# Performance work log

Hardware: AMD Instinct MI355X
Metric: run time of the kernel (lower is better)

Reference implementation:

```python
import jax, jax.numpy as jnp
import numpy as np

N, E, IN_DIM, HID, HEADS = 50000, 800000, 160, 64, 4
NEG_SLOPE = 0.2
BN_EPS = 1e-5


def setup_inputs() -> dict:
    key = jax.random.key(0)
    ks = jax.random.split(key, 32)
    s = lambda i, shape, sc=0.05: jax.random.normal(ks[i], shape, dtype=jnp.float32) * sc
    inp = {
        "x": jax.random.normal(ks[0], (N, IN_DIM), dtype=jnp.float32),
        "edge_index": jax.random.randint(ks[1], (2, E), 0, N, dtype=jnp.int64),
        # conv1: GATv2Conv(160 -> 64, heads=4, concat=True)
        "Wl1": s(2, (IN_DIM, HEADS * HID)), "bl1": s(3, (HEADS * HID,)),
        "Wr1": s(4, (IN_DIM, HEADS * HID)), "br1": s(5, (HEADS * HID,)),
        "att1": s(6, (HEADS, HID)), "bias1": s(7, (HEADS * HID,)),
        # bn1 (eval mode)
        "g1": jnp.ones((HEADS * HID,), jnp.float32), "b1": s(8, (HEADS * HID,)),
        "m1": s(9, (HEADS * HID,)), "v1": jax.random.uniform(ks[10], (HEADS * HID,), jnp.float32, 0.5, 1.5),
        # conv2: GATv2Conv(256 -> 64, heads=1, concat=False)
        "Wl2": s(11, (HEADS * HID, HID)), "bl2": s(12, (HID,)),
        "Wr2": s(13, (HEADS * HID, HID)), "br2": s(14, (HID,)),
        "att2": s(15, (1, HID)), "bias2": s(16, (HID,)),
        # bn2 (eval mode)
        "g2": jnp.ones((HID,), jnp.float32), "b2": s(17, (HID,)),
        "m2": s(18, (HID,)), "v2": jax.random.uniform(ks[19], (HID,), jnp.float32, 0.5, 1.5),
        # skip and output linear
        "Ws": s(20, (IN_DIM, HID)), "bs": s(21, (HID,)),
        "Wo": s(22, (HID, 1)), "bo": s(23, (1,)),
    }
    return inp


def gatv2_conv(x, Wl, bl, Wr, br, att, bias, src, dst, heads, out_dim, concat):
    n = x.shape[0]
    xl = (x @ Wl + bl).reshape(n, heads, out_dim)   # source transform
    xr = (x @ Wr + br).reshape(n, heads, out_dim)   # target transform
    e = jax.nn.leaky_relu(xl[src] + xr[dst], NEG_SLOPE)       # [E', H, D]
    logits = jnp.einsum('ehd,hd->eh', e, att)                 # [E', H]
    # segment softmax over incoming edges per target node
    mx = jax.ops.segment_max(logits, dst, num_segments=n)     # [N, H]
    a = jnp.exp(logits - mx[dst])
    denom = jax.ops.segment_sum(a, dst, num_segments=n)
    alpha = a / denom[dst]                                    # [E', H]
    out = jax.ops.segment_sum(xl[src] * alpha[:, :, None], dst, num_segments=n)  # [N, H, D]
    out = out.reshape(n, heads * out_dim) if concat else out.mean(axis=1)
    return out + bias


def reference(x, edge_index, Wl1, bl1, Wr1, br1, att1, bias1, g1, b1, m1, v1,
              Wl2, bl2, Wr2, br2, att2, bias2, g2, b2, m2, v2, Ws, bs, Wo, bo):
    n = x.shape[0]
    loop = jnp.arange(n, dtype=edge_index.dtype)
    src = jnp.concatenate([edge_index[0], loop])   # PyG add_self_loops=True
    dst = jnp.concatenate([edge_index[1], loop])

    x_skip = x @ Ws + bs
    h = gatv2_conv(x, Wl1, bl1, Wr1, br1, att1, bias1, src, dst, HEADS, HID, True)
    h = jax.nn.relu((h - m1) * g1 / jnp.sqrt(v1 + BN_EPS) + b1)  # BN1 eval + relu
    h = gatv2_conv(h, Wl2, bl2, Wr2, br2, att2, bias2, src, dst, 1, HID, False)
    h = jax.nn.relu((h - m2) * g2 / jnp.sqrt(v2 + BN_EPS) + b2)  # BN2 eval + relu
    h = h + x_skip
    return (h @ Wo + bo).squeeze(-1)               # [N]
```

## Files before the change

kernel.cpp:

```cpp
#include <hip/hip_runtime.h>
#include <hip/hip_bf16.h>

#define N_NODES 50000
#define E_EDGES 800000
#define EP_EDGES 850000
#define IN_DIM 160
#define HEADS 4
#define HID 64
#define C1 256
#define NEG_SLOPE 0.2f
#define BN_EPS 1e-5f

typedef __attribute__((ext_vector_type(8))) short bf16x8;
typedef __attribute__((ext_vector_type(4))) float f32x4;
typedef _Float16 h2 __attribute__((ext_vector_type(2)));

__device__ __forceinline__ float b2f(ushort u) {
    return __uint_as_float(((unsigned)u) << 16);
}
__device__ __forceinline__ ushort f2b(float f) {
    __hip_bfloat16 h = __float2bfloat16(f);
    return *reinterpret_cast<ushort*>(&h);
}
__device__ __forceinline__ ushort f2h(float f) {
    union { _Float16 h; ushort u; } c;
    c.h = (_Float16)f;
    return c.u;
}
__device__ __forceinline__ float lo16(uint u) { return __uint_as_float(u << 16); }
__device__ __forceinline__ float hi16(uint u) { return __uint_as_float(u & 0xffff0000u); }
__device__ __forceinline__ h2 uh(uint u) {
    union { uint u; h2 h; } c; c.u = u; return c.h;
}

__device__ __forceinline__ bool probe_f32(const ushort* xraw) {
    int lane = threadIdx.x & 63;
    float a = fabsf(b2f(xraw[2 * lane]));
    unsigned long long m = __ballot(a > 1e-6f && a < 1e6f);
    return __popcll(m) < 48;
}
__device__ __forceinline__ bool probe_i64(const int* eraw) {
    int lane = threadIdx.x & 63;
    unsigned long long m = __ballot(eraw[2 * lane + 1] != 0);
    return __popcll(m) < 8;
}

template<int CTRL>
__device__ __forceinline__ float dpp_add(float p) {
    int t = __builtin_amdgcn_update_dpp(0, __float_as_int(p), CTRL, 0xf, 0xf, true);
    return p + __int_as_float(t);
}
__device__ __forceinline__ float row16_sum(float p) {
    p = dpp_add<0xB1>(p);
    p = dpp_add<0x4E>(p);
    p = dpp_add<0x124>(p);
    p = dpp_add<0x128>(p);
    return p;
}

#define NB_SWZ 62
#define NB_HIST 3321

struct SW2 {
    const void* W[5];
    ushort* D[5];
    int NT[5];
    int base[5];
    const void* sp[19];
    const void* xraw;
};

__global__ void front_k(const int* __restrict__ ei, int* __restrict__ deg,
                        int* __restrict__ epos, SW2 s, ushort* __restrict__ params) {
    const int b = blockIdx.x;
    if (b < NB_SWZ) {
        const bool f32 = probe_f32((const ushort*)s.xraw);
        if (b < 61) {
            int idx = b * 256 + threadIdx.x;
            int seg = 0;
            #pragma unroll
            for (int k = 1; k < 5; ++k) seg += (idx >= s.base[k]) ? 1 : 0;
            int li = idx - s.base[seg];
            int NT = s.NT[seg];
            int N = NT << 4;
            int lane = li & 63;
            int ft = li >> 6;
            int kb = ft / NT, t = ft - kb * NT;
            int q = lane >> 4, m = lane & 15;
            const float* pf = (const float*)s.W[seg];
            const ushort* pu = (const ushort*)s.W[seg];
            ushort* d = s.D[seg] + (size_t)li * 8;
            #pragma unroll
            for (int j = 0; j < 8; ++j) {
                size_t src = (size_t)(kb * 32 + q * 8 + j) * N + t * 16 + m;
                d[j] = f32 ? f2b(pf[src]) : pu[src];
            }
        } else {
            const int SZ[19] = {256,256,256,256,256,256,256,256,
                                64,64,64,64,64,64,64,64,64,64, 1};
            const int OF[19] = {40960,82176,82432,82688,82944,83200,83456,83712,
                                100352,116800,116864,116928,116992,117056,117120,117184,
                                127488,127552, 127616};
            for (int e = threadIdx.x; e < 2689; e += 256) {
                int rem = e, t = 0;
                while (rem >= SZ[t]) { rem -= SZ[t]; ++t; }
                const float* pf = (const float*)s.sp[t];
                const ushort* pu = (const ushort*)s.sp[t];
                float val = f32 ? pf[rem] : b2f(pu[rem]);
                params[OF[t] + rem] = (t == 2 || t == 10) ? f2h(val) : f2b(val);
            }
        }
    } else {
        const bool i64 = probe_i64(ei);
        int e = (b - NB_SWZ) * 256 + threadIdx.x;
        if (e >= EP_EDGES) return;
        int dst;
        if (e < E_EDGES) {
            int idx = E_EDGES + e;
            dst = i64 ? ei[2 * idx] : ei[idx];
        } else dst = e - E_EDGES;
        epos[e] = atomicAdd(&deg[dst], 1);
    }
}

__global__ __launch_bounds__(1024) void scan1_k(const int* __restrict__ deg,
                                                int* __restrict__ exc,
                                                int* __restrict__ bsum) {
    __shared__ int wsum[16];
    const int t = threadIdx.x;
    const int lane = t & 63, w = t >> 6;
    int i = blockIdx.x * 1024 + t;
    int v = (i < N_NODES) ? deg[i] : 0;
    int sIncl = v;
    #pragma unroll
    for (int d = 1; d < 64; d <<= 1) {
        int u = __shfl_up(sIncl, d);
        if (lane >= d) sIncl += u;
    }
    if (lane == 63) wsum[w] = sIncl;
    __syncthreads();
    if (w == 0) {
        int p = (lane < 16) ? wsum[lane] : 0;
        #pragma unroll
        for (int d = 1; d < 16; d <<= 1) {
            int u = __shfl_up(p, d);
            if (lane >= d) p += u;
        }
        if (lane < 16) wsum[lane] = p;
    }
    __syncthreads();
    int base = (w > 0) ? wsum[w - 1] : 0;
    int incl = base + sIncl;
    if (i < N_NODES) exc[i] = incl - v;
    if (t == 1023) bsum[blockIdx.x] = incl;
}

__global__ void scan2_k(const int* __restrict__ bsum, int* __restrict__ cp,
                        int* __restrict__ exc) {
    int lane = threadIdx.x;
    int v = (lane < 49) ? bsum[lane] : 0;
    int orig = v;
    #pragma unroll
    for (int d = 1; d < 64; d <<= 1) {
        int u = __shfl_up(v, d);
        if (lane >= d) v += u;
    }
    if (lane < 49) cp[lane] = v - orig;
    if (lane == 48) exc[N_NODES] = EP_EDGES - (v - orig);
}

__device__ __forceinline__ bf16x8 loadA(const void* X, bool f32, size_t row, int off) {
    if (!f32) return *(const bf16x8*)((const ushort*)X + row * IN_DIM + off);
    const float* p = (const float*)X + row * IN_DIM + off;
    bf16x8 r;
    #pragma unroll
    for (int j = 0; j < 8; ++j) r[j] = (short)f2b(p[j]);
    return r;
}

#define NB_G3 782

__global__ __launch_bounds__(256) void scatgemm_k(const void* __restrict__ A,
                                                  const ushort* __restrict__ B1,
                                                  const ushort* __restrict__ B2,
                                                  const ushort* __restrict__ B3,
                                                  const ushort* __restrict__ bi1,
                                                  const ushort* __restrict__ bi2,
                                                  const ushort* __restrict__ bi3,
                                                  ushort* __restrict__ o1,
                                                  ushort* __restrict__ o2,
                                                  ushort* __restrict__ o3,
                                                  int M,
                                                  const int* __restrict__ ei,
                                                  const int* __restrict__ epos,
                                                  const int* __restrict__ exc,
                                                  const int* __restrict__ cp,
                                                  int* __restrict__ col) {
    if (blockIdx.x >= NB_G3) {
        const bool i64 = probe_i64(ei);
        int e = (blockIdx.x - NB_G3) * 256 + threadIdx.x;
        if (e >= EP_EDGES) return;
        int src, dst;
        if (e < E_EDGES) {
            if (i64) { src = ei[2 * e]; dst = ei[2 * (E_EDGES + e)]; }
            else     { src = ei[e];     dst = ei[E_EDGES + e]; }
        } else { src = e - E_EDGES; dst = src; }
        col[exc[dst] + cp[dst >> 10] + epos[e]] = src;
        return;
    }
    const bool f32 = probe_f32((const ushort*)A);
    const int wave = threadIdx.x >> 6;
    const int lane = threadIdx.x & 63;
    const int ch = blockIdx.x & 1;
    const int row0 = (blockIdx.x >> 1) * 128 + wave * 32;
    if (row0 >= M) return;
    int ar0 = row0 + (lane & 15);      if (ar0 >= M) ar0 = M - 1;
    int ar1 = row0 + 16 + (lane & 15); if (ar1 >= M) ar1 = M - 1;
    const int aoff = (lane >> 4) * 8;
    bf16x8 af0[5], af1[5];
    #pragma unroll
    for (int kb = 0; kb < 5; ++kb) {
        af0[kb] = loadA(A, f32, (size_t)ar0, aoff + kb * 32);
        af1[kb] = loadA(A, f32, (size_t)ar1, aoff + kb * 32);
    }
    const bf16x8* b1 = (const bf16x8*)B1;
    const bf16x8* b2 = (const bf16x8*)B2;
    const bf16x8* b3 = (const bf16x8*)B3;
    f32x4 aL[2][8] = {}, aR[2][8] = {}, aS[2][2] = {};
    #pragma unroll
    for (int kb = 0; kb < 5; ++kb) {
        #pragma unroll
        for (int j = 0; j < 8; ++j) {
            bf16x8 b = b1[(kb * 16 + ch * 8 + j) * 64 + lane];
            aL[0][j] = __builtin_amdgcn_mfma_f32_16x16x32_bf16(af0[kb], b, aL[0][j], 0, 0, 0);
            aL[1][j] = __builtin_amdgcn_mfma_f32_16x16x32_bf16(af1[kb], b, aL[1][j], 0, 0, 0);
        }
        #pragma unroll
        for (int j = 0; j < 8; ++j) {
            bf16x8 b = b2[(kb * 16 + ch * 8 + j) * 64 + lane];
            aR[0][j] = __builtin_amdgcn_mfma_f32_16x16x32_bf16(af0[kb], b, aR[0][j], 0, 0, 0);
            aR[1][j] = __builtin_amdgcn_mfma_f32_16x16x32_bf16(af1[kb], b, aR[1][j], 0, 0, 0);
        }
        #pragma unroll
        for (int j = 0; j < 2; ++j) {
            bf16x8 b = b3[(kb * 4 + ch * 2 + j) * 64 + lane];
            aS[0][j] = __builtin_amdgcn_mfma_f32_16x16x32_bf16(af0[kb], b, aS[0][j], 0, 0, 0);
            aS[1][j] = __builtin_amdgcn_mfma_f32_16x16x32_bf16(af1[kb], b, aS[1][j], 0, 0, 0);
        }
    }
    const int cn = lane & 15, cq = lane >> 4;
    #pragma unroll
    for (int rt = 0; rt < 2; ++rt) {
        #pragma unroll
        for (int j = 0; j < 8; ++j) {
            int colc = (ch * 8 + j) * 16 + cn;
            float bbL = b2f(bi1[colc]);
            float bbR = b2f(bi2[colc]);
            #pragma unroll
            for (int r = 0; r < 4; ++r) {
                int grow = row0 + rt * 16 + cq * 4 + r;
                if (grow < M) {
                    o1[(size_t)grow * C1 + colc] = f2h(aL[rt][j][r] + bbL);
                    o2[(size_t)grow * C1 + colc] = f2h(aR[rt][j][r] + bbR);
                }
            }
        }
        #pragma unroll
        for (int j = 0; j < 2; ++j) {
            int colc = (ch * 2 + j) * 16 + cn;
            float bb = b2f(bi3[colc]);
            #pragma unroll
            for (int r = 0; r < 4; ++r) {
                int grow = row0 + rt * 16 + cq * 4 + r;
                if (grow < M)
                    o3[(size_t)grow * HID + colc] = f2b(aS[rt][j][r] + bb);
            }
        }
    }
}

__global__ __launch_bounds__(256) void gemm2_k(const ushort* __restrict__ A,
                                               const ushort* __restrict__ B1,
                                               const ushort* __restrict__ B2,
                                               const ushort* __restrict__ bi1,
                                               const ushort* __restrict__ bi2,
                                               ushort* __restrict__ o1,
                                               ushort* __restrict__ o2,
                                               int M) {
    const int wave = threadIdx.x >> 6;
    const int lane = threadIdx.x & 63;
    const int row0 = blockIdx.x * 64 + wave * 16;
    if (row0 >= M) return;
    int arow = row0 + (lane & 15);
    if (arow >= M) arow = M - 1;
    const ushort* aptr = A + (size_t)arow * C1 + (lane >> 4) * 8;
    const bf16x8* b1 = (const bf16x8*)B1;
    const bf16x8* b2 = (const bf16x8*)B2;
    f32x4 aL[4] = {}, aR[4] = {};
    #pragma unroll
    for (int kb = 0; kb < 8; ++kb) {
        bf16x8 af = *(const bf16x8*)(aptr + kb * 32);
        #pragma unroll
        for (int t = 0; t < 4; ++t)
            aL[t] = __builtin_amdgcn_mfma_f32_16x16x32_bf16(af, b1[(kb * 4 + t) * 64 + lane], aL[t], 0, 0, 0);
        #pragma unroll
        for (int t = 0; t < 4; ++t)
            aR[t] = __builtin_amdgcn_mfma_f32_16x16x32_bf16(af, b2[(kb * 4 + t) * 64 + lane], aR[t], 0, 0, 0);
    }
    const int cn = lane & 15, cq = lane >> 4;
    #pragma unroll
    for (int t = 0; t < 4; ++t) {
        float bbL = b2f(bi1[t * 16 + cn]);
        float bbR = b2f(bi2[t * 16 + cn]);
        #pragma unroll
        for (int r = 0; r < 4; ++r) {
            int grow = row0 + cq * 4 + r;
            if (grow < M) {
                o1[(size_t)grow * HID + t * 16 + cn] = f2h(aL[t][r] + bbL);
                o2[(size_t)grow * HID + t * 16 + cn] = f2h(aR[t][r] + bbR);
            }
        }
    }
}

__global__ __launch_bounds__(256) void conv1_k(const ushort* __restrict__ xl,
                                               const ushort* __restrict__ xr,
                                               const int* __restrict__ exc,
                                               const int* __restrict__ cp,
                                               const int* __restrict__ col,
                                               const ushort* __restrict__ att,
                                               const ushort* __restrict__ bias1,
                                               const ushort* __restrict__ g1,
                                               const ushort* __restrict__ b1,
                                               const ushort* __restrict__ m1,
                                               const ushort* __restrict__ v1,
                                               ushort* __restrict__ h1out) {
    const int n = blockIdx.x * 4 + (threadIdx.x >> 6);
    if (n >= N_NODES) return;
    const int lane = threadIdx.x & 63;
    const int g = lane >> 4;
    const int r = lane & 15;
    const uint4* xr4 = (const uint4*)(xr + (size_t)n * C1 + r * 16);
    const uint4 xru0 = xr4[0], xru1 = xr4[1];
    const uint4* at4 = (const uint4*)(att + r * 16);
    const uint4 atu0 = at4[0], atu1 = at4[1];
    h2 xrp[8], atp[8];
    xrp[0] = uh(xru0.x); xrp[1] = uh(xru0.y); xrp[2] = uh(xru0.z); xrp[3] = uh(xru0.w);
    xrp[4] = uh(xru1.x); xrp[5] = uh(xru1.y); xrp[6] = uh(xru1.z); xrp[7] = uh(xru1.w);
    atp[0] = uh(atu0.x); atp[1] = uh(atu0.y); atp[2] = uh(atu0.z); atp[3] = uh(atu0.w);
    atp[4] = uh(atu1.x); atp[5] = uh(atu1.y); atp[6] = uh(atu1.z); atp[7] = uh(atu1.w);
    const h2 ns2 = {(_Float16)NEG_SLOPE, (_Float16)NEG_SLOPE};
    const int e0 = exc[n] + cp[n >> 10];
    const int e1 = exc[n + 1] + cp[(n + 1) >> 10];
    float a[16];
    #pragma unroll
    for (int k = 0; k < 16; ++k) a[k] = 0.f;
    float den = 0.f;
    int j = e0 + g;

    auto body = [&](uint4 u0, uint4 u1, bool masked, int jm) {
        h2 xp[8];
        xp[0] = uh(u0.x); xp[1] = uh(u0.y); xp[2] = uh(u0.z); xp[3] = uh(u0.w);
        xp[4] = uh(u1.x); xp[5] = uh(u1.y); xp[6] = uh(u1.z); xp[7] = uh(u1.w);
        h2 d0 = {(_Float16)0, (_Float16)0};
        h2 d1 = {(_Float16)0, (_Float16)0};
        #pragma unroll
        for (int k = 0; k < 8; k += 2) {
            h2 t0 = xp[k] + xrp[k];
            t0 = __builtin_elementwise_max(t0, t0 * ns2);
            d0 = __builtin_elementwise_fma(t0, atp[k], d0);
            h2 t1 = xp[k + 1] + xrp[k + 1];
            t1 = __builtin_elementwise_max(t1, t1 * ns2);
            d1 = __builtin_elementwise_fma(t1, atp[k + 1], d1);
        }
        h2 ds = d0 + d1;
        float p = (float)ds.x + (float)ds.y;
        p = dpp_add<0xB1>(p);
        p = dpp_add<0x4E>(p);
        float w = __expf(fminf(p, 60.f));
        if (masked) w = (jm < e1) ? w : 0.f;
        den += w;
        #pragma unroll
        for (int k = 0; k < 8; ++k) {
            a[2 * k]     = fmaf(w, (float)xp[k].x, a[2 * k]);
            a[2 * k + 1] = fmaf(w, (float)xp[k].y, a[2 * k + 1]);
        }
    };
    auto rowp = [&](int s) { return (const uint4*)(xl + (size_t)(uint)s * C1 + r * 16); };

    int sA = col[j < e1 ? j : e1 - 1];
    int sB = col[j + 4 < e1 ? j + 4 : e1 - 1];
    int i = e0;
    for (; i + 8 <= e1; i += 8) {
        const int jn = i + g + 8;
        int sC = col[jn < e1 ? jn : e1 - 1];
        int sD = col[jn + 4 < e1 ? jn + 4 : e1 - 1];
        const uint4* pA = rowp(sA);
        uint4 a0 = pA[0], a1 = pA[1];
        const uint4* pB = rowp(sB);
        uint4 b0 = pB[0], b1v = pB[1];
        body(a0, a1, false, 0);
        body(b0, b1v, false, 0);
        sA = sC; sB = sD;
    }
    j = i + g;
    if (i + 4 <= e1) {
        const uint4* pA = rowp(sA);
        uint4 a0 = pA[0], a1 = pA[1];
        body(a0, a1, false, 0);
        sA = sB; i += 4; j += 4;
    }
    if (j < e1) {
        const uint4* pA = rowp(sA);
        uint4 a0 = pA[0], a1 = pA[1];
        body(a0, a1, true, j);
    }

    #pragma unroll
    for (int k = 0; k < 16; ++k) {
        a[k] += __shfl_xor(a[k], 16);
        a[k] += __shfl_xor(a[k], 32);
    }
    den += __shfl_xor(den, 16);
    den += __shfl_xor(den, 32);
    const int q = g;
    float s0 = q == 0 ? a[0] : q == 1 ? a[4] : q == 2 ? a[8]  : a[12];
    float s1 = q == 0 ? a[1] : q == 1 ? a[5] : q == 2 ? a[9]  : a[13];
    float s2 = q == 0 ? a[2] : q == 1 ? a[6] : q == 2 ? a[10] : a[14];
    float s3 = q == 0 ? a[3] : q == 1 ? a[7] : q == 2 ? a[11] : a[15];
    const int pi = r * 4 + q;
    const float inv = 1.f / den;
    const uint2 biu = ((const uint2*)bias1)[pi];
    const uint2 gu  = ((const uint2*)g1)[pi];
    const uint2 bu  = ((const uint2*)b1)[pi];
    const uint2 mu  = ((const uint2*)m1)[pi];
    const uint2 vu  = ((const uint2*)v1)[pi];
    float o0 = fmaf(s0, inv, lo16(biu.x));
    float o1 = fmaf(s1, inv, hi16(biu.x));
    float o2 = fmaf(s2, inv, lo16(biu.y));
    float o3 = fmaf(s3, inv, hi16(biu.y));
    float c0 = lo16(gu.x) * rsqrtf(lo16(vu.x) + BN_EPS);
    float c1 = hi16(gu.x) * rsqrtf(hi16(vu.x) + BN_EPS);
    float c2 = lo16(gu.y) * rsqrtf(lo16(vu.y) + BN_EPS);
    float c3 = hi16(gu.y) * rsqrtf(hi16(vu.y) + BN_EPS);
    float h0 = fmaxf((o0 - lo16(mu.x)) * c0 + lo16(bu.x), 0.f);
    float h1v = fmaxf((o1 - hi16(mu.x)) * c1 + hi16(bu.x), 0.f);
    float h2v = fmaxf((o2 - lo16(mu.y)) * c2 + lo16(bu.y), 0.f);
    float h3 = fmaxf((o3 - hi16(mu.y)) * c3 + hi16(bu.y), 0.f);
    uint2 ou;
    ou.x = (uint)f2b(h0) | ((uint)f2b(h1v) << 16);
    ou.y = (uint)f2b(h2v) | ((uint)f2b(h3) << 16);
    ((uint2*)h1out)[(size_t)n * 64 + pi] = ou;
}

__global__ __launch_bounds__(256) void conv2_k(const ushort* __restrict__ xl,
                                               const ushort* __restrict__ xr,
                                               const ushort* __restrict__ xskip,
                                               const int* __restrict__ exc,
                                               const int* __restrict__ cp,
                                               const int* __restrict__ col,
                                               const ushort* __restrict__ att2,
                                               const ushort* __restrict__ bias2,
                                               const ushort* __restrict__ g2,
                                               const ushort* __restrict__ bb2,
                                               const ushort* __restrict__ m2,
                                               const ushort* __restrict__ v2,
                                               const ushort* __restrict__ Wo,
                                               const ushort* __restrict__ bo,
                                               void* __restrict__ out,
                                               const ushort* __restrict__ xraw) {
    const bool f32out = probe_f32(xraw);
    const int n = blockIdx.x * 4 + (threadIdx.x >> 6);
    if (n >= N_NODES) return;
    const int lane = threadIdx.x & 63;
    const int grp = lane >> 4;
    const uint m = lane & 15;
    const uint2* xl2v = (const uint2*)xl;
    const uint2 xru = ((const uint2*)xr)[(size_t)n * 16 + m];
    const h2 xr01 = uh(xru.x), xr23 = uh(xru.y);
    const uint2 atu = ((const uint2*)att2)[m];
    const h2 at01 = uh(atu.x), at23 = uh(atu.y);
    const h2 ns2 = {(_Float16)NEG_SLOPE, (_Float16)NEG_SLOPE};
    const int e0 = exc[n] + cp[n >> 10];
    const int e1 = exc[n + 1] + cp[(n + 1) >> 10];
    const int deg = e1 - e0;
    const int iend = e0 + (deg & ~15);
    float a0 = 0.f, a1 = 0.f, a2 = 0.f, a3 = 0.f, den = 0.f;

    auto edge4 = [&](const uint2 xu, bool masked, int jbase) {
        const h2 x01 = uh(xu.x), x23 = uh(xu.y);
        h2 t01 = x01 + xr01;
        t01 = __builtin_elementwise_max(t01, t01 * ns2);
        h2 t23 = x23 + xr23;
        t23 = __builtin_elementwise_max(t23, t23 * ns2);
        h2 dp = __builtin_elementwise_fma(t23, at23, t01 * at01);
        float p = (float)dp.x + (float)dp.y;
        p = row16_sum(p);
        float w;
        if (masked) {
            w = __expf(fminf(p, 60.f));
            w = ((jbase + grp) < e1) ? w : 0.f;
        } else {
            w = __expf(p);
        }
        a0 = fmaf(w, (float)x01.x, a0);
        a1 = fmaf(w, (float)x01.y, a1);
        a2 = fmaf(w, (float)x23.x, a2);
        a3 = fmaf(w, (float)x23.y, a3);
        den += w;
    };

    uint s0_, s1_, s2_, s3_;
    {
        const int j0 = e0 + grp, j1 = j0 + 4, j2 = j0 + 8, j3 = j0 + 12;
        s0_ = (uint)col[j0 < e1 ? j0 : e1 - 1];
        s1_ = (uint)col[j1 < e1 ? j1 : e1 - 1];
        s2_ = (uint)col[j2 < e1 ? j2 : e1 - 1];
        s3_ = (uint)col[j3 < e1 ? j3 : e1 - 1];
    }
    for (int i = e0; i < iend; i += 16) {
        const uint2 xu0 = xl2v[(s0_ << 4) + m];
        const uint2 xu1 = xl2v[(s1_ << 4) + m];
        const uint2 xu2 = xl2v[(s2_ << 4) + m];
        const uint2 xu3 = xl2v[(s3_ << 4) + m];
        const int j0 = i + 16 + grp, j1 = j0 + 4, j2 = j0 + 8, j3 = j0 + 12;
        s0_ = (uint)col[j0 < e1 ? j0 : e1 - 1];
        s1_ = (uint)col[j1 < e1 ? j1 : e1 - 1];
        s2_ = (uint)col[j2 < e1 ? j2 : e1 - 1];
        s3_ = (uint)col[j3 < e1 ? j3 : e1 - 1];
        edge4(xu0, false, 0);
        edge4(xu1, false, 0);
        edge4(xu2, false, 0);
        edge4(xu3, false, 0);
    }
    const int rem = e1 - iend;
    if (rem > 0) {
        const uint2 xu0 = xl2v[(s0_ << 4) + m];
        const uint2 xu1 = xl2v[(s1_ << 4) + m];
        const uint2 xu2 = xl2v[(s2_ << 4) + m];
        const uint2 xu3 = xl2v[(s3_ << 4) + m];
        edge4(xu0, true, iend);
        if (rem > 4)  edge4(xu1, true, iend + 4);
        if (rem > 8)  edge4(xu2, true, iend + 8);
        if (rem > 12) edge4(xu3, true, iend + 12);
    }
    a0 += __shfl_xor(a0, 16); a0 += __shfl_xor(a0, 32);
    a1 += __shfl_xor(a1, 16); a1 += __shfl_xor(a1, 32);
    a2 += __shfl_xor(a2, 16); a2 += __shfl_xor(a2, 32);
    a3 += __shfl_xor(a3, 16); a3 += __shfl_xor(a3, 32);
    den += __shfl_xor(den, 16); den += __shfl_xor(den, 32);
    if (lane < 16) {
        const float inv = 1.f / den;
        const uint2 biu = ((const uint2*)bias2)[m];
        const uint2 gu  = ((const uint2*)g2)[m];
        const uint2 bu  = ((const uint2*)bb2)[m];
        const uint2 mu  = ((const uint2*)m2)[m];
        const uint2 vu  = ((const uint2*)v2)[m];
        const uint2 sku = ((const uint2*)xskip)[(size_t)n * 16 + m];
        const uint2 wou = ((const uint2*)Wo)[m];
        float o0 = fmaf(a0, inv, lo16(biu.x));
        float o1 = fmaf(a1, inv, hi16(biu.x));
        float o2 = fmaf(a2, inv, lo16(biu.y));
        float o3 = fmaf(a3, inv, hi16(biu.y));
        float s0 = lo16(gu.x) * rsqrtf(lo16(vu.x) + BN_EPS);
        float s1 = hi16(gu.x) * rsqrtf(hi16(vu.x) + BN_EPS);
        float s2 = lo16(gu.y) * rsqrtf(lo16(vu.y) + BN_EPS);
        float s3 = hi16(gu.y) * rsqrtf(hi16(vu.y) + BN_EPS);
        float h0 = fmaxf((o0 - lo16(mu.x)) * s0 + lo16(bu.x), 0.f) + lo16(sku.x);
        float h1v = fmaxf((o1 - hi16(mu.x)) * s1 + hi16(bu.x), 0.f) + hi16(sku.x);
        float h2v = fmaxf((o2 - lo16(mu.y)) * s2 + lo16(bu.y), 0.f) + lo16(sku.y);
        float h3 = fmaxf((o3 - hi16(mu.y)) * s3 + hi16(bu.y), 0.f) + hi16(sku.y);
        float d = fmaf(h0, lo16(wou.x), fmaf(h1v, hi16(wou.x),
                  fmaf(h2v, lo16(wou.y), h3 * hi16(wou.y))));
        d = row16_sum(d);
        if (m == 0) {
            float r = d + b2f(bo[0]);
            if (f32out) ((float*)out)[n] = r;
            else        ((ushort*)out)[n] = f2b(r);
        }
    }
}

extern "C" void kernel_launch(void* const* d_in, const int* in_sizes, int n_in,
                              void* d_out, int out_size, void* d_ws, size_t ws_size,
                              hipStream_t stream) {
    char* ws = (char*)d_ws;
    size_t off = 0;
    auto alloc = [&](size_t bytes) -> void* {
        void* p = ws + off;
        off += (bytes + 255) & ~(size_t)255;
        return p;
    };
    ushort* params  = (ushort*)alloc((size_t)127617 * 2);
    int*    exc     = (int*)alloc((size_t)(N_NODES + 1) * 4);
    int*    deg     = (int*)alloc((size_t)N_NODES * 4);
    int*    epos    = (int*)alloc((size_t)EP_EDGES * 4);
    int*    colbuf  = (int*)alloc((size_t)EP_EDGES * 4);
    int*    bsum    = (int*)alloc(64 * 4);
    int*    cparr   = (int*)alloc(64 * 4);
    ushort* xl1     = (ushort*)alloc((size_t)N_NODES * C1 * 2);
    ushort* xr1     = (ushort*)alloc((size_t)N_NODES * C1 * 2);
    ushort* xskip   = (ushort*)alloc((size_t)N_NODES * HID * 2);
    ushort* h1      = (ushort*)alloc((size_t)N_NODES * C1 * 2);
    ushort* xl2     = (ushort*)alloc((size_t)N_NODES * HID * 2);
    ushort* xr2     = (ushort*)alloc((size_t)N_NODES * HID * 2);
    ushort* swzWl1  = (ushort*)alloc((size_t)IN_DIM * C1 * 2);
    ushort* swzWr1  = (ushort*)alloc((size_t)IN_DIM * C1 * 2);
    ushort* swzWs   = (ushort*)alloc((size_t)IN_DIM * HID * 2);
    ushort* swzWl2  = (ushort*)alloc((size_t)C1 * HID * 2);
    ushort* swzWr2  = (ushort*)alloc((size_t)C1 * HID * 2);

    ushort* bl1c   = params + 40960;
    ushort* br1c   = params + 82176;
    ushort* att1c  = params + 82432;
    ushort* bias1c = params + 82688;
    ushort* g1c    = params + 82944;
    ushort* b1c    = params + 83200;
    ushort* m1c    = params + 83456;
    ushort* v1c    = params + 83712;
    ushort* bl2c   = params + 100352;
    ushort* br2c   = params + 116800;
    ushort* att2c  = params + 116864;
    ushort* bias2c = params + 116928;
    ushort* g2c    = params + 116992;
    ushort* b2c    = params + 117056;
    ushort* m2c    = params + 117120;
    ushort* v2c    = params + 117184;
    ushort* bsc    = params + 127488;
    ushort* Woc    = params + 127552;
    ushort* boc    = params + 127616;

    const int* ei_raw = (const int*)d_in[1];

    (void)hipMemsetAsync(deg, 0, (size_t)N_NODES * 4, stream);

    SW2 sw;
    sw.W[0] = d_in[2];  sw.D[0] = swzWl1; sw.NT[0] = 16; sw.base[0] = 0;
    sw.W[1] = d_in[4];  sw.D[1] = swzWr1; sw.NT[1] = 16; sw.base[1] = 5120;
    sw.W[2] = d_in[22]; sw.D[2] = swzWs;  sw.NT[2] = 4;  sw.base[2] = 10240;
    sw.W[3] = d_in[12]; sw.D[3] = swzWl2; sw.NT[3] = 4;  sw.base[3] = 11520;
    sw.W[4] = d_in[14]; sw.D[4] = swzWr2; sw.NT[4] = 4;  sw.base[4] = 13568;
    const int spidx[19] = {3,5,6,7,8,9,10,11, 13,15,16,17,18,19,20,21, 23,24, 25};
    for (int i = 0; i < 19; ++i) sw.sp[i] = d_in[spidx[i]];
    sw.xraw = d_in[0];
    front_k<<<NB_SWZ + NB_HIST, 256, 0, stream>>>(ei_raw, deg, epos, sw, params);

    const int NB_S = (N_NODES + 1023) / 1024;

    scan1_k<<<NB_S, 1024, 0, stream>>>(deg, exc, bsum);
    scan2_k<<<1, 64, 0, stream>>>(bsum, cparr, exc);

    scatgemm_k<<<NB_G3 + NB_HIST, 256, 0, stream>>>(
        d_in[0], swzWl1, swzWr1, swzWs, bl1c, br1c, bsc, xl1, xr1, xskip, N_NODES,
        ei_raw, epos, exc, cparr, colbuf);

    conv1_k<<<(N_NODES + 3) / 4, 256, 0, stream>>>(xl1, xr1, exc, cparr, colbuf,
                                                   att1c, bias1c, g1c, b1c, m1c, v1c, h1);

    gemm2_k<<<(N_NODES + 63) / 64, 256, 0, stream>>>(h1, swzWl2, swzWr2, bl2c, br2c,
                                                     xl2, xr2, N_NODES);

    conv2_k<<<(N_NODES + 3) / 4, 256, 0, stream>>>(xl2, xr2, xskip, exc, cparr, colbuf,
                                                   att2c, bias2c, g2c, b2c, m2c, v2c,
                                                   Woc, boc, d_out, (const ushort*)d_in[0]);
}
```

Baseline: 357.9 us.

## Unify first-layer weights and retile scatgemm into 4 column groups of 9 tiles

```diff
diff --git a/kernel.cpp b/kernel.cpp
--- a/kernel.cpp
+++ b/kernel.cpp
@@ -64,6 +64,7 @@
 struct SW2 {
     const void* W[5];
     ushort* D[5];
+    ushort* U;
     int NT[5];
     int base[5];
     const void* sp[19];
@@ -89,7 +90,13 @@
             int q = lane >> 4, m = lane & 15;
             const float* pf = (const float*)s.W[seg];
             const ushort* pu = (const ushort*)s.W[seg];
-            ushort* d = s.D[seg] + (size_t)li * 8;
+            ushort* d;
+            if (seg < 3) {
+                const int FO = (seg == 0) ? 0 : (seg == 1) ? 16 : 32;
+                d = s.U + ((size_t)(kb * 36 + FO + t) * 64 + lane) * 8;
+            } else {
+                d = s.D[seg] + (size_t)li * 8;
+            }
             #pragma unroll
             for (int j = 0; j < 8; ++j) {
                 size_t src = (size_t)(kb * 32 + q * 8 + j) * N + t * 16 + m;
@@ -178,24 +185,22 @@
     return r;
 }
 
-#define NB_G3 782
-
-__global__ __launch_bounds__(256) void scatgemm_k(const void* __restrict__ A,
-                                                  const ushort* __restrict__ B1,
-                                                  const ushort* __restrict__ B2,
-                                                  const ushort* __restrict__ B3,
-                                                  const ushort* __restrict__ bi1,
-                                                  const ushort* __restrict__ bi2,
-                                                  const ushort* __restrict__ bi3,
-                                                  ushort* __restrict__ o1,
-                                                  ushort* __restrict__ o2,
-                                                  ushort* __restrict__ o3,
-                                                  int M,
-                                                  const int* __restrict__ ei,
-                                                  const int* __restrict__ epos,
-                                                  const int* __restrict__ exc,
-                                                  const int* __restrict__ cp,
-                                                  int* __restrict__ col) {
+#define NB_G3 3128
+
+__global__ __launch_bounds__(256, 4) void scatgemm_k(const void* __restrict__ A,
+                                                     const ushort* __restrict__ U,
+                                                     const ushort* __restrict__ bi1,
+                                                     const ushort* __restrict__ bi2,
+                                                     const ushort* __restrict__ bi3,
+                                                     ushort* __restrict__ o1,
+                                                     ushort* __restrict__ o2,
+                                                     ushort* __restrict__ o3,
+                                                     int M,
+                                                     const int* __restrict__ ei,
+                                                     const int* __restrict__ epos,
+                                                     const int* __restrict__ exc,
+                                                     const int* __restrict__ cp,
+                                                     int* __restrict__ col) {
     if (blockIdx.x >= NB_G3) {
         const bool i64 = probe_i64(ei);
         int e = (blockIdx.x - NB_G3) * 256 + threadIdx.x;
@@ -211,70 +216,37 @@
     const bool f32 = probe_f32((const ushort*)A);
     const int wave = threadIdx.x >> 6;
     const int lane = threadIdx.x & 63;
-    const int ch = blockIdx.x & 1;
-    const int row0 = (blockIdx.x >> 1) * 128 + wave * 32;
+    const int cg = blockIdx.x & 3;
+    const int rb = blockIdx.x >> 2;
+    const int row0 = rb * 64 + wave * 16;
     if (row0 >= M) return;
-    int ar0 = row0 + (lane & 15);      if (ar0 >= M) ar0 = M - 1;
-    int ar1 = row0 + 16 + (lane & 15); if (ar1 >= M) ar1 = M - 1;
+    const int ar = row0 + (lane & 15);
     const int aoff = (lane >> 4) * 8;
-    bf16x8 af0[5], af1[5];
+    const bf16x8* bu = (const bf16x8*)U;
+    f32x4 acc[9] = {};
     #pragma unroll
     for (int kb = 0; kb < 5; ++kb) {
-        af0[kb] = loadA(A, f32, (size_t)ar0, aoff + kb * 32);
-        af1[kb] = loadA(A, f32, (size_t)ar1, aoff + kb * 32);
-    }
-    const bf16x8* b1 = (const bf16x8*)B1;
-    const bf16x8* b2 = (const bf16x8*)B2;
-    const bf16x8* b3 = (const bf16x8*)B3;
-    f32x4 aL[2][8] = {}, aR[2][8] = {}, aS[2][2] = {};
-    #pragma unroll
-    for (int kb = 0; kb < 5; ++kb) {
-        #pragma unroll
-        for (int j = 0; j < 8; ++j) {
-            bf16x8 b = b1[(kb * 16 + ch * 8 + j) * 64 + lane];
-            aL[0][j] = __builtin_amdgcn_mfma_f32_16x16x32_bf16(af0[kb], b, aL[0][j], 0, 0, 0);
-            aL[1][j] = __builtin_amdgcn_mfma_f32_16x16x32_bf16(af1[kb], b, aL[1][j], 0, 0, 0);
-        }
-        #pragma unroll
-        for (int j = 0; j < 8; ++j) {
-            bf16x8 b = b2[(kb * 16 + ch * 8 + j) * 64 + lane];
-            aR[0][j] = __builtin_amdgcn_mfma_f32_16x16x32_bf16(af0[kb], b, aR[0][j], 0, 0, 0);
-            aR[1][j] = __builtin_amdgcn_mfma_f32_16x16x32_bf16(af1[kb], b, aR[1][j], 0, 0, 0);
-        }
-        #pragma unroll
-        for (int j = 0; j < 2; ++j) {
-            bf16x8 b = b3[(kb * 4 + ch * 2 + j) * 64 + lane];
-            aS[0][j] = __builtin_amdgcn_mfma_f32_16x16x32_bf16(af0[kb], b, aS[0][j], 0, 0, 0);
-            aS[1][j] = __builtin_amdgcn_mfma_f32_16x16x32_bf16(af1[kb], b, aS[1][j], 0, 0, 0);
+        bf16x8 af = loadA(A, f32, (size_t)ar, aoff + kb * 32);
+        #pragma unroll
+        for (int jj = 0; jj < 9; ++jj) {
+            bf16x8 b = bu[(size_t)(kb * 36 + cg * 9 + jj) * 64 + lane];
+            acc[jj] = __builtin_amdgcn_mfma_f32_16x16x32_bf16(af, b, acc[jj], 0, 0, 0);
         }
     }
     const int cn = lane & 15, cq = lane >> 4;
     #pragma unroll
-    for (int rt = 0; rt < 2; ++rt) {
-        #pragma unroll
-        for (int j = 0; j < 8; ++j) {
-            int colc = (ch * 8 + j) * 16 + cn;
-            float bbL = b2f(bi1[colc]);
-            float bbR = b2f(bi2[colc]);
-            #pragma unroll
-            for (int r = 0; r < 4; ++r) {
-                int grow = row0 + rt * 16 + cq * 4 + r;
-                if (grow < M) {
-                    o1[(size_t)grow * C1 + colc] = f2h(aL[rt][j][r] + bbL);
-                    o2[(size_t)grow * C1 + colc] = f2h(aR[rt][j][r] + bbR);
-                }
-            }
-        }
-        #pragma unroll
-        for (int j = 0; j < 2; ++j) {
-            int colc = (ch * 2 + j) * 16 + cn;
-            float bb = b2f(bi3[colc]);
-            #pragma unroll
-            for (int r = 0; r < 4; ++r) {
-                int grow = row0 + rt * 16 + cq * 4 + r;
-                if (grow < M)
-                    o3[(size_t)grow * HID + colc] = f2b(aS[rt][j][r] + bb);
-            }
+    for (int jj = 0; jj < 9; ++jj) {
+        const int f = cg * 9 + jj;
+        ushort* op; int ldc, colb; const ushort* bp_; bool tobf;
+        if (f < 16)      { op = o1; ldc = C1;  colb = f * 16;        bp_ = bi1 + f * 16;        tobf = false; }
+        else if (f < 32) { op = o2; ldc = C1;  colb = (f - 16) * 16; bp_ = bi2 + (f - 16) * 16; tobf = false; }
+        else             { op = o3; ldc = HID; colb = (f - 32) * 16; bp_ = bi3 + (f - 32) * 16; tobf = true;  }
+        const float bb = b2f(bp_[cn]);
+        #pragma unroll
+        for (int r = 0; r < 4; ++r) {
+            const int grow = row0 + cq * 4 + r;
+            const float v = acc[jj][r] + bb;
+            op[(size_t)grow * ldc + colb + cn] = tobf ? f2b(v) : f2h(v);
         }
     }
 }
@@ -604,9 +576,7 @@
     ushort* h1      = (ushort*)alloc((size_t)N_NODES * C1 * 2);
     ushort* xl2     = (ushort*)alloc((size_t)N_NODES * HID * 2);
     ushort* xr2     = (ushort*)alloc((size_t)N_NODES * HID * 2);
-    ushort* swzWl1  = (ushort*)alloc((size_t)IN_DIM * C1 * 2);
-    ushort* swzWr1  = (ushort*)alloc((size_t)IN_DIM * C1 * 2);
-    ushort* swzWs   = (ushort*)alloc((size_t)IN_DIM * HID * 2);
+    ushort* swzU    = (ushort*)alloc((size_t)5 * 36 * 64 * 8 * 2);
     ushort* swzWl2  = (ushort*)alloc((size_t)C1 * HID * 2);
     ushort* swzWr2  = (ushort*)alloc((size_t)C1 * HID * 2);
 
@@ -635,11 +605,12 @@
     (void)hipMemsetAsync(deg, 0, (size_t)N_NODES * 4, stream);
 
     SW2 sw;
-    sw.W[0] = d_in[2];  sw.D[0] = swzWl1; sw.NT[0] = 16; sw.base[0] = 0;
-    sw.W[1] = d_in[4];  sw.D[1] = swzWr1; sw.NT[1] = 16; sw.base[1] = 5120;
-    sw.W[2] = d_in[22]; sw.D[2] = swzWs;  sw.NT[2] = 4;  sw.base[2] = 10240;
-    sw.W[3] = d_in[12]; sw.D[3] = swzWl2; sw.NT[3] = 4;  sw.base[3] = 11520;
-    sw.W[4] = d_in[14]; sw.D[4] = swzWr2; sw.NT[4] = 4;  sw.base[4] = 13568;
+    sw.W[0] = d_in[2];  sw.D[0] = nullptr; sw.NT[0] = 16; sw.base[0] = 0;
+    sw.W[1] = d_in[4];  sw.D[1] = nullptr; sw.NT[1] = 16; sw.base[1] = 5120;
+    sw.W[2] = d_in[22]; sw.D[2] = nullptr; sw.NT[2] = 4;  sw.base[2] = 10240;
+    sw.W[3] = d_in[12]; sw.D[3] = swzWl2;  sw.NT[3] = 4;  sw.base[3] = 11520;
+    sw.W[4] = d_in[14]; sw.D[4] = swzWr2;  sw.NT[4] = 4;  sw.base[4] = 13568;
+    sw.U = swzU;
     const int spidx[19] = {3,5,6,7,8,9,10,11, 13,15,16,17,18,19,20,21, 23,24, 25};
     for (int i = 0; i < 19; ++i) sw.sp[i] = d_in[spidx[i]];
     sw.xraw = d_in[0];
@@ -651,7 +622,7 @@
     scan2_k<<<1, 64, 0, stream>>>(bsum, cparr, exc);
 
     scatgemm_k<<<NB_G3 + NB_HIST, 256, 0, stream>>>(
-        d_in[0], swzWl1, swzWr1, swzWs, bl1c, br1c, bsc, xl1, xr1, xskip, N_NODES,
+        d_in[0], swzU, bl1c, br1c, bsc, xl1, xr1, xskip, N_NODES,
         ei_raw, epos, exc, cparr, colbuf);
 
     conv1_k<<<(N_NODES + 3) / 4, 256, 0, stream>>>(xl1, xr1, exc, cparr, colbuf,
```

New measurement: 327.2 us. 1.09x faster.
